# Optimization experiments

Hardware: AMD Instinct MI355X
Metric: run time of the kernel (lower is better)

Reference implementation:

```python
import jax, jax.numpy as jnp
import numpy as np

N_NODES = 10000
N_EDGES = 320000
IN_DIM = 512
HID = 128


def setup_inputs() -> dict:
    key = jax.random.key(0)
    k1, k2, k3, k4 = jax.random.split(key, 4)
    x = jax.random.normal(k1, (N_NODES, IN_DIM), dtype=jnp.float32)
    edge_index = jax.random.randint(k2, (2, N_EDGES), 0, N_NODES, dtype=jnp.int64)
    W_enc = jax.random.normal(k3, (IN_DIM, HID), dtype=jnp.float32) * 0.05
    b_enc = jnp.zeros((HID,), dtype=jnp.float32)
    W_dec = jax.random.normal(k4, (HID, N_NODES), dtype=jnp.float32) * 0.05
    b_dec = jnp.zeros((N_NODES,), dtype=jnp.float32)
    return {"x": x, "edge_index": edge_index, "W_enc": W_enc, "b_enc": b_enc,
            "W_dec": W_dec, "b_dec": b_dec}


def reference(x, edge_index, W_enc, b_enc, W_dec, b_dec):
    N = x.shape[0]
    # ---- GCNConv (PyG defaults: self-loops + symmetric normalization) ----
    h = x @ W_enc                                  # [N, HID]
    loops = jnp.arange(N, dtype=edge_index.dtype)
    src = jnp.concatenate([edge_index[0], loops])  # source j
    dst = jnp.concatenate([edge_index[1], loops])  # target i
    ones = jnp.ones(src.shape[0], dtype=h.dtype)
    deg = jax.ops.segment_sum(ones, dst, num_segments=N)          # in-degree incl. self-loop
    dinv = jnp.where(deg > 0, jax.lax.rsqrt(deg), 0.0)
    norm = dinv[src] * dinv[dst]                                   # [E+N]
    msgs = h[src] * norm[:, None]                                  # gather-scale
    agg = jax.ops.segment_sum(msgs, dst, num_segments=N)           # scatter-add [N, HID]
    encoded = agg + b_enc
    # ---- decoder: Linear + sigmoid ----
    decoded = jax.nn.sigmoid(encoded @ W_dec + b_dec)              # [N, N]
    return decoded
```

## Files before the change

### kernel.cpp

```cpp
#include <hip/hip_runtime.h>
#include <hip/hip_bf16.h>

#define N_NODES 10000
#define IN_DIM 512
#define HID 128
#define MP 10112
#define NPAD 10240

typedef __attribute__((ext_vector_type(8))) __bf16 bf16x8;
typedef __attribute__((ext_vector_type(8))) unsigned short u16x8;
typedef __attribute__((ext_vector_type(4))) float f32x4;

__device__ __forceinline__ unsigned short f2bf(float f) {
    unsigned int u = __float_as_uint(f);
    return (unsigned short)((u + 0x7fffu + ((u >> 16) & 1u)) >> 16);
}

__global__ void k_zero_cnt(int* cnt) {
    int i = blockIdx.x * 256 + threadIdx.x;
    if (i < NPAD) cnt[i] = 0;
}

__global__ void k_hist(const int* __restrict__ ei, int* cnt, int E) {
    int e = blockIdx.x * 256 + threadIdx.x;
    if (e < E) atomicAdd(&cnt[ei[E + e]], 1);
}

__global__ void k_scan(const int* __restrict__ cnt, int* __restrict__ base,
                       int* __restrict__ cursor, float* __restrict__ dinv) {
    __shared__ int lds[256];
    int t = threadIdx.x;
    int loc[40];
    int sum = 0;
#pragma unroll
    for (int j = 0; j < 40; ++j) {
        int idx = t * 40 + j;
        int c = cnt[idx];
        loc[j] = sum;
        sum += c;
    }
    lds[t] = sum;
    __syncthreads();
    for (int off = 1; off < 256; off <<= 1) {
        int v = (t >= off) ? lds[t - off] : 0;
        __syncthreads();
        lds[t] += v;
        __syncthreads();
    }
    int ex = lds[t] - sum;
#pragma unroll
    for (int j = 0; j < 40; ++j) {
        int idx = t * 40 + j;
        int b = ex + loc[j];
        base[idx] = b;
        cursor[idx] = b;
        dinv[idx] = rsqrtf((float)cnt[idx] + 1.0f);
    }
}

__global__ void k_fill(const int* __restrict__ ei, const float* __restrict__ dinv,
                       int* cursor, int2* __restrict__ csr, int E) {
    int e = blockIdx.x * 256 + threadIdx.x;
    if (e >= E) return;
    int s = ei[e];
    int d = ei[E + e];
    int pos = atomicAdd(&cursor[d], 1);
    float w = dinv[s] * dinv[d];
    csr[pos] = make_int2(s, __float_as_int(w));
}

__global__ void k_cast_wenc(const float* __restrict__ w, __hip_bfloat16* __restrict__ wT) {
    int idx = blockIdx.x * 256 + threadIdx.x;
    int n = idx & (HID - 1);
    int k = idx >> 7;
    wT[n * IN_DIM + k] = __float2bfloat16(w[k * HID + n]);
}

__global__ __launch_bounds__(256) void k_wdec_t(const float* __restrict__ wdec,
                                                __hip_bfloat16* __restrict__ wT) {
    __shared__ float tile[32][33];
    int tx = threadIdx.x, ty = threadIdx.y;
    int n0 = blockIdx.x * 32, k0 = blockIdx.y * 32;
#pragma unroll
    for (int j = 0; j < 4; ++j) {
        int k = k0 + ty * 4 + j;
        int n = n0 + tx;
        tile[ty * 4 + j][tx] = (n < N_NODES) ? wdec[(size_t)k * N_NODES + n] : 0.0f;
    }
    __syncthreads();
#pragma unroll
    for (int j = 0; j < 4; ++j) {
        int n = n0 + ty * 4 + j;
        int k = k0 + tx;
        wT[(size_t)n * HID + k] = __float2bfloat16(tile[tx][ty * 4 + j]);
    }
}

__global__ __launch_bounds__(256) void k_enc_gemm(
    const float* __restrict__ x, const __hip_bfloat16* __restrict__ wencT,
    float* __restrict__ h)
{
    int tid = threadIdx.x;
    int wv = tid >> 6, lane = tid & 63;
    int l16 = lane & 15, quad = lane >> 4;
    int m_w = blockIdx.x * 32 + (wv >> 1) * 16;
    int n_w = (wv & 1) * 64;
    f32x4 acc[4] = {};
    int row = m_w + l16;
    bool rv = row < N_NODES;
    const float* xr = x + (size_t)row * IN_DIM;
    for (int kk = 0; kk < IN_DIM; kk += 32) {
        int k0 = kk + quad * 8;
        f32x4 u = {}, w = {};
        if (rv) {
            u = *(const f32x4*)(xr + k0);
            w = *(const f32x4*)(xr + k0 + 4);
        }
        union { u16x8 u; bf16x8 v; } a;
#pragma unroll
        for (int j = 0; j < 4; ++j) {
            a.u[j] = f2bf(u[j]);
            a.u[4 + j] = f2bf(w[j]);
        }
        bf16x8 b[4];
#pragma unroll
        for (int ni = 0; ni < 4; ++ni)
            b[ni] = *(const bf16x8*)(const void*)(wencT + (size_t)(n_w + ni * 16 + l16) * IN_DIM + k0);
#pragma unroll
        for (int ni = 0; ni < 4; ++ni)
            acc[ni] = __builtin_amdgcn_mfma_f32_16x16x32_bf16(a.v, b[ni], acc[ni], 0, 0, 0);
    }
#pragma unroll
    for (int ni = 0; ni < 4; ++ni) {
        int n = n_w + ni * 16 + l16;
#pragma unroll
        for (int r = 0; r < 4; ++r) {
            int m = m_w + quad * 4 + r;
            if (m < N_NODES) h[(size_t)m * HID + n] = acc[ni][r];
        }
    }
}

__global__ __launch_bounds__(128) void k_agg_enc(
    const float* __restrict__ h, const int2* __restrict__ csr,
    const int* __restrict__ base, const int* __restrict__ cnt,
    const float* __restrict__ dinv, const float* __restrict__ b_enc,
    __hip_bfloat16* __restrict__ enc)
{
    int i = blockIdx.x;
    int t = threadIdx.x;
    if (i >= N_NODES) {
        enc[(size_t)i * HID + t] = __float2bfloat16(0.0f);
        return;
    }
    float di = dinv[i];
    float acc0 = di * di * h[(size_t)i * HID + t];
    float acc1 = 0.0f;
    int j0 = base[i], d = cnt[i];
    int half = d >> 1;
    int mid = j0 + half;
    for (int off = 0; off < half; ++off) {
        int2 p0 = csr[j0 + off];
        int2 p1 = csr[mid + off];
        acc0 += __int_as_float(p0.y) * h[(size_t)p0.x * HID + t];
        acc1 += __int_as_float(p1.y) * h[(size_t)p1.x * HID + t];
    }
    if (d & 1) {
        int2 p = csr[j0 + d - 1];
        acc1 += __int_as_float(p.y) * h[(size_t)p.x * HID + t];
    }
    enc[(size_t)i * HID + t] = __float2bfloat16(acc0 + acc1 + b_enc[t]);
}

__global__ __launch_bounds__(256) void k_dec_gemm(
    const __hip_bfloat16* __restrict__ A, const __hip_bfloat16* __restrict__ BT,
    const float* __restrict__ bias, float* __restrict__ C)
{
    const int NT = 79;
    const int nwg = NT * NT;
    const int q = nwg >> 3, rr = nwg & 7;
    int orig = blockIdx.x;
    int xcd = orig & 7, lin = orig >> 3;
    int wg = (xcd < rr ? xcd * (q + 1) : rr * (q + 1) + (xcd - rr) * q) + lin;
    int bx = wg % NT;
    int by = wg / NT;

    int tid = threadIdx.x;
    int wv = tid >> 6, lane = tid & 63;
    int l16 = lane & 15, quad = lane >> 4;
    int m_w = by * 128 + (wv >> 1) * 64;
    int n_w = bx * 128 + (wv & 1) * 64;

    f32x4 acc[4][4] = {};
    for (int kk = 0; kk < HID; kk += 32) {
        int k0 = kk + quad * 8;
        bf16x8 a[4], b[4];
#pragma unroll
        for (int mi = 0; mi < 4; ++mi)
            a[mi] = *(const bf16x8*)(const void*)(A + (size_t)(m_w + mi * 16 + l16) * HID + k0);
#pragma unroll
        for (int ni = 0; ni < 4; ++ni)
            b[ni] = *(const bf16x8*)(const void*)(BT + (size_t)(n_w + ni * 16 + l16) * HID + k0);
#pragma unroll
        for (int mi = 0; mi < 4; ++mi)
#pragma unroll
            for (int ni = 0; ni < 4; ++ni)
                acc[mi][ni] = __builtin_amdgcn_mfma_f32_16x16x32_bf16(b[ni], a[mi], acc[mi][ni], 0, 0, 0);
    }
#pragma unroll
    for (int mi = 0; mi < 4; ++mi) {
        int m = m_w + mi * 16 + l16;
        if (m >= N_NODES) continue;
        size_t rowoff = (size_t)m * N_NODES;
#pragma unroll
        for (int ni = 0; ni < 4; ++ni) {
            int n4 = n_w + ni * 16 + quad * 4;
            if (n4 >= N_NODES) continue;
            f32x4 bv = *(const f32x4*)(bias + n4);
            f32x4 z = acc[mi][ni];
            f32x4 s;
#pragma unroll
            for (int r = 0; r < 4; ++r) {
                float e = __expf(-(z[r] + bv[r]));
                s[r] = __builtin_amdgcn_rcpf(1.0f + e);
            }
            *(f32x4*)(C + rowoff + n4) = s;
        }
    }
}

extern "C" void kernel_launch(void* const* d_in, const int* in_sizes, int n_in,
                              void* d_out, int out_size, void* d_ws, size_t ws_size,
                              hipStream_t stream) {
    const float* x     = (const float*)d_in[0];
    const int*   ei    = (const int*)d_in[1];
    const float* W_enc = (const float*)d_in[2];
    const float* b_enc = (const float*)d_in[3];
    const float* W_dec = (const float*)d_in[4];
    const float* b_dec = (const float*)d_in[5];
    float* out = (float*)d_out;
    const int E = in_sizes[1] / 2;

    char* p = (char*)d_ws;
    auto carve = [&](size_t bytes) -> char* {
        char* r = p;
        p += (bytes + 255) & ~(size_t)255;
        return r;
    };
    int*   cnt    = (int*)carve((size_t)NPAD * 4);
    int*   base   = (int*)carve((size_t)NPAD * 4);
    int*   cursor = (int*)carve((size_t)NPAD * 4);
    float* dinv   = (float*)carve((size_t)NPAD * 4);
    int2*  csr    = (int2*)carve((size_t)E * 8);
    float* h      = (float*)carve((size_t)N_NODES * HID * 4);
    __hip_bfloat16* wencT = (__hip_bfloat16*)carve((size_t)HID * IN_DIM * 2);
    __hip_bfloat16* encb  = (__hip_bfloat16*)carve((size_t)MP * HID * 2);
    __hip_bfloat16* wdecT = (__hip_bfloat16*)carve((size_t)MP * HID * 2);

    k_zero_cnt<<<dim3(NPAD / 256), dim3(256), 0, stream>>>(cnt);
    k_hist<<<dim3((E + 255) / 256), dim3(256), 0, stream>>>(ei, cnt, E);
    k_scan<<<dim3(1), dim3(256), 0, stream>>>(cnt, base, cursor, dinv);
    k_fill<<<dim3((E + 255) / 256), dim3(256), 0, stream>>>(ei, dinv, cursor, csr, E);

    k_cast_wenc<<<dim3(HID * IN_DIM / 256), dim3(256), 0, stream>>>(W_enc, wencT);
    k_wdec_t<<<dim3(MP / 32, HID / 32), dim3(32, 8), 0, stream>>>(W_dec, wdecT);

    k_enc_gemm<<<dim3((N_NODES + 31) / 32), dim3(256), 0, stream>>>(x, wencT, h);

    k_agg_enc<<<dim3(MP), dim3(128), 0, stream>>>(h, csr, base, cnt, dinv, b_enc, encb);

    k_dec_gemm<<<dim3(79 * 79), dim3(256), 0, stream>>>(encb, wdecT, b_dec, out);
}
```

Baseline: 618.4 us.

## Stage decoder GEMM tiles in LDS with 256x256 blocks and swizzle

The decoder GEMM now uses 256x256 output tiles per 512-thread workgroup. The full K=128 slices of A and B are loaded into 128KB of LDS with direct global-to-LDS loads and an XOR swizzle to avoid bank conflicts, replacing the previous direct global fragment loads on 128x128 tiles. The aggregation kernel is also widened to four independent accumulators to expose more memory-level parallelism on the neighbor gathers. Padding moves to 10240 rows to match the new tile size. The large LDS footprint limits occupancy to one workgroup per CU, and the output store, which writes a 400MB float matrix, likely dominates anyway.

```diff
diff --git a/kernel.cpp b/kernel.cpp
--- a/kernel.cpp
+++ b/kernel.cpp
@@ -4,7 +4,6 @@
 #define N_NODES 10000
 #define IN_DIM 512
 #define HID 128
-#define MP 10112
 #define NPAD 10240
 
 typedef __attribute__((ext_vector_type(8))) __bf16 bf16x8;
@@ -14,6 +13,12 @@
 __device__ __forceinline__ unsigned short f2bf(float f) {
     unsigned int u = __float_as_uint(f);
     return (unsigned short)((u + 0x7fffu + ((u >> 16) & 1u)) >> 16);
+}
+
+__device__ __forceinline__ void gload_lds16(const void* g, void* l) {
+    __builtin_amdgcn_global_load_lds(
+        (const __attribute__((address_space(1))) unsigned int*)g,
+        (__attribute__((address_space(3))) unsigned int*)l, 16, 0, 0);
 }
 
 __global__ void k_zero_cnt(int* cnt) {
@@ -154,61 +159,93 @@
         return;
     }
     float di = dinv[i];
-    float acc0 = di * di * h[(size_t)i * HID + t];
-    float acc1 = 0.0f;
+    float a0 = di * di * h[(size_t)i * HID + t];
+    float a1 = 0.0f, a2 = 0.0f, a3 = 0.0f;
     int j0 = base[i], d = cnt[i];
-    int half = d >> 1;
-    int mid = j0 + half;
-    for (int off = 0; off < half; ++off) {
-        int2 p0 = csr[j0 + off];
-        int2 p1 = csr[mid + off];
-        acc0 += __int_as_float(p0.y) * h[(size_t)p0.x * HID + t];
-        acc1 += __int_as_float(p1.y) * h[(size_t)p1.x * HID + t];
-    }
-    if (d & 1) {
-        int2 p = csr[j0 + d - 1];
-        acc1 += __int_as_float(p.y) * h[(size_t)p.x * HID + t];
-    }
-    enc[(size_t)i * HID + t] = __float2bfloat16(acc0 + acc1 + b_enc[t]);
-}
-
-__global__ __launch_bounds__(256) void k_dec_gemm(
+    int q4 = d >> 2;
+    const int2* c0 = csr + j0;
+    const int2* c1 = c0 + q4;
+    const int2* c2 = c1 + q4;
+    const int2* c3 = c2 + q4;
+    for (int off = 0; off < q4; ++off) {
+        int2 p0 = c0[off], p1 = c1[off], p2 = c2[off], p3 = c3[off];
+        a0 += __int_as_float(p0.y) * h[(size_t)p0.x * HID + t];
+        a1 += __int_as_float(p1.y) * h[(size_t)p1.x * HID + t];
+        a2 += __int_as_float(p2.y) * h[(size_t)p2.x * HID + t];
+        a3 += __int_as_float(p3.y) * h[(size_t)p3.x * HID + t];
+    }
+    for (int j = j0 + (q4 << 2); j < j0 + d; ++j) {
+        int2 p = csr[j];
+        a0 += __int_as_float(p.y) * h[(size_t)p.x * HID + t];
+    }
+    enc[(size_t)i * HID + t] = __float2bfloat16(((a0 + a1) + (a2 + a3)) + b_enc[t]);
+}
+
+__global__ __launch_bounds__(512) void k_dec_gemm(
     const __hip_bfloat16* __restrict__ A, const __hip_bfloat16* __restrict__ BT,
     const float* __restrict__ bias, float* __restrict__ C)
 {
-    const int NT = 79;
-    const int nwg = NT * NT;
-    const int q = nwg >> 3, rr = nwg & 7;
+    extern __shared__ char lds[];
+    char* ldsA = lds;
+    char* ldsB = lds + 65536;
+
+    const int NT = 40;
     int orig = blockIdx.x;
-    int xcd = orig & 7, lin = orig >> 3;
-    int wg = (xcd < rr ? xcd * (q + 1) : rr * (q + 1) + (xcd - rr) * q) + lin;
-    int bx = wg % NT;
-    int by = wg / NT;
+    int wg = (orig & 7) * 200 + (orig >> 3);
+    int bx = wg % NT, by = wg / NT;
 
     int tid = threadIdx.x;
     int wv = tid >> 6, lane = tid & 63;
     int l16 = lane & 15, quad = lane >> 4;
-    int m_w = by * 128 + (wv >> 1) * 64;
-    int n_w = bx * 128 + (wv & 1) * 64;
-
-    f32x4 acc[4][4] = {};
-    for (int kk = 0; kk < HID; kk += 32) {
-        int k0 = kk + quad * 8;
-        bf16x8 a[4], b[4];
-#pragma unroll
-        for (int mi = 0; mi < 4; ++mi)
-            a[mi] = *(const bf16x8*)(const void*)(A + (size_t)(m_w + mi * 16 + l16) * HID + k0);
-#pragma unroll
-        for (int ni = 0; ni < 4; ++ni)
-            b[ni] = *(const bf16x8*)(const void*)(BT + (size_t)(n_w + ni * 16 + l16) * HID + k0);
-#pragma unroll
-        for (int mi = 0; mi < 4; ++mi)
+    int wm = wv >> 2, wn = wv & 3;
+
+    {
+        const char* gA = (const char*)A + (size_t)by * 65536;
+        const char* gB = (const char*)BT + (size_t)bx * 65536;
+        int wb = wv * 1024;
+#pragma unroll
+        for (int it = 0; it < 8; ++it) {
+            int L = wb + it * 8192 + lane * 16;
+            int row = L >> 8;
+            int src = (row << 8) | ((L & 255) ^ ((row & 7) << 4));
+            gload_lds16(gA + src, ldsA + wb + it * 8192);
+        }
+#pragma unroll
+        for (int it = 0; it < 8; ++it) {
+            int L = wb + it * 8192 + lane * 16;
+            int row = L >> 8;
+            int src = (row << 8) | ((L & 255) ^ ((row & 7) << 4));
+            gload_lds16(gB + src, ldsB + wb + it * 8192);
+        }
+    }
+    asm volatile("s_waitcnt vmcnt(0)" ::: "memory");
+    __syncthreads();
+
+    f32x4 acc[8][4] = {};
+    int qb = quad * 16;
+#pragma unroll
+    for (int ks = 0; ks < 4; ++ks) {
+        int kb = ks * 64 + qb;
+        bf16x8 b[4];
+#pragma unroll
+        for (int ni = 0; ni < 4; ++ni) {
+            int r = wn * 64 + ni * 16 + l16;
+            b[ni] = *(const bf16x8*)(ldsB + ((r << 8) + (kb ^ ((r & 7) << 4))));
+        }
+#pragma unroll
+        for (int mi = 0; mi < 8; ++mi) {
+            int r = wm * 128 + mi * 16 + l16;
+            bf16x8 a = *(const bf16x8*)(ldsA + ((r << 8) + (kb ^ ((r & 7) << 4))));
 #pragma unroll
             for (int ni = 0; ni < 4; ++ni)
-                acc[mi][ni] = __builtin_amdgcn_mfma_f32_16x16x32_bf16(b[ni], a[mi], acc[mi][ni], 0, 0, 0);
-    }
-#pragma unroll
-    for (int mi = 0; mi < 4; ++mi) {
+                acc[mi][ni] = __builtin_amdgcn_mfma_f32_16x16x32_bf16(b[ni], a, acc[mi][ni], 0, 0, 0);
+        }
+    }
+
+    int m_w = by * 256 + wm * 128;
+    int n_w = bx * 256 + wn * 64;
+#pragma unroll
+    for (int mi = 0; mi < 8; ++mi) {
         int m = m_w + mi * 16 + l16;
         if (m >= N_NODES) continue;
         size_t rowoff = (size_t)m * N_NODES;
@@ -254,8 +291,8 @@
     int2*  csr    = (int2*)carve((size_t)E * 8);
     float* h      = (float*)carve((size_t)N_NODES * HID * 4);
     __hip_bfloat16* wencT = (__hip_bfloat16*)carve((size_t)HID * IN_DIM * 2);
-    __hip_bfloat16* encb  = (__hip_bfloat16*)carve((size_t)MP * HID * 2);
-    __hip_bfloat16* wdecT = (__hip_bfloat16*)carve((size_t)MP * HID * 2);
+    __hip_bfloat16* encb  = (__hip_bfloat16*)carve((size_t)NPAD * HID * 2);
+    __hip_bfloat16* wdecT = (__hip_bfloat16*)carve((size_t)NPAD * HID * 2);
 
     k_zero_cnt<<<dim3(NPAD / 256), dim3(256), 0, stream>>>(cnt);
     k_hist<<<dim3((E + 255) / 256), dim3(256), 0, stream>>>(ei, cnt, E);
@@ -263,11 +300,11 @@
     k_fill<<<dim3((E + 255) / 256), dim3(256), 0, stream>>>(ei, dinv, cursor, csr, E);
 
     k_cast_wenc<<<dim3(HID * IN_DIM / 256), dim3(256), 0, stream>>>(W_enc, wencT);
-    k_wdec_t<<<dim3(MP / 32, HID / 32), dim3(32, 8), 0, stream>>>(W_dec, wdecT);
+    k_wdec_t<<<dim3(NPAD / 32, HID / 32), dim3(32, 8), 0, stream>>>(W_dec, wdecT);
 
     k_enc_gemm<<<dim3((N_NODES + 31) / 32), dim3(256), 0, stream>>>(x, wencT, h);
 
-    k_agg_enc<<<dim3(MP), dim3(128), 0, stream>>>(h, csr, base, cnt, dinv, b_enc, encb);
-
-    k_dec_gemm<<<dim3(79 * 79), dim3(256), 0, stream>>>(encb, wdecT, b_dec, out);
-}
+    k_agg_enc<<<dim3(NPAD), dim3(128), 0, stream>>>(h, csr, base, cnt, dinv, b_enc, encb);
+
+    k_dec_gemm<<<dim3(40 * 40), dim3(512), 131072, stream>>>(encb, wdecT, b_dec, out);
+}
```

After: 559.5 us. 1.11x faster.
